# Kernel optimization log

Hardware: AMD Instinct MI355X
Metric: run time of the kernel (lower is better)

## Reference

```python
import jax, jax.numpy as jnp
import numpy as np

N, E, H, NH = 10000, 160000, 128, 8
HD = H // NH
LDIM = 8  # (lmax+1)**2 - 1 with lmax=2
CUTOFF = 5.0


def setup_inputs() -> dict:
    key = jax.random.key(0)
    ks = jax.random.split(key, 20)
    w = lambda k, shape: jax.random.normal(k, shape, jnp.float32) * 0.05
    return dict(
        node_feats=jax.random.normal(ks[0], (N, H), jnp.float32),
        edge_feats=jax.random.normal(ks[1], (E, H), jnp.float32),
        vector_feats=jax.random.normal(ks[2], (N, LDIM, H), jnp.float32),
        distances=jax.random.uniform(ks[3], (E,), jnp.float32) * CUTOFF,
        d_ij=jax.random.normal(ks[4], (E, LDIM), jnp.float32),
        senders=jax.random.randint(ks[5], (E,), 0, N),
        receivers=jax.random.randint(ks[6], (E,), 0, N),
        ln_scale=jnp.ones((H,), jnp.float32),
        ln_bias=jnp.zeros((H,), jnp.float32),
        vln_w=jnp.ones((H,), jnp.float32),
        W_vec=w(ks[7], (H, 3 * H)),
        Wq=w(ks[8], (H, H)), bq=jnp.zeros((H,), jnp.float32),
        Wk=w(ks[9], (H, H)), bk=jnp.zeros((H,), jnp.float32),
        Wv=w(ks[10], (H, H)), bv=jnp.zeros((H,), jnp.float32),
        Wdk=w(ks[11], (H, H)), bdk=jnp.zeros((H,), jnp.float32),
        Wdv=w(ks[12], (H, H)), bdv=jnp.zeros((H,), jnp.float32),
        Ws=w(ks[13], (H, 2 * H)), bs=jnp.zeros((2 * H,), jnp.float32),
        Wo=w(ks[14], (H, 3 * H)), bo=jnp.zeros((3 * H,), jnp.float32),
        Wf=w(ks[15], (H, H)), bf=jnp.zeros((H,), jnp.float32),
        Wsrc=w(ks[16], (H, H)),
        Wtrg=w(ks[17], (H, H)),
    )


def _reject(vec, d):
    # vector rejection of vec [E, L, H] against direction d [E, L]
    proj = (vec * d[:, :, None]).sum(axis=1, keepdims=True)
    return vec - proj * d[:, :, None]


def _forward(node_feats, edge_feats, vector_feats, distances, d_ij, senders, receivers,
             ln_scale, ln_bias, vln_w, W_vec, Wq, bq, Wk, bk, Wv, bv, Wdk, bdk, Wdv, bdv,
             Ws, bs, Wo, bo, Wf, bf, Wsrc, Wtrg):
    silu = jax.nn.silu
    n = node_feats.shape[0]
    # LayerNorm (eps=1e-5) on node feats
    mu = node_feats.mean(-1, keepdims=True)
    xc = node_feats - mu
    var = (xc * xc).mean(-1, keepdims=True)
    x = xc * jax.lax.rsqrt(var + 1e-5) * ln_scale + ln_bias
    # VecLayerNorm with norm_type='none' -> identity norm + learned per-channel scale
    vec = vector_feats * vln_w
    q = (x @ Wq + bq).reshape(-1, NH, HD)
    k = (x @ Wk + bk).reshape(-1, NH, HD)
    v = (x @ Wv + bv).reshape(-1, NH, HD)
    dk = silu(edge_feats @ Wdk + bdk).reshape(-1, NH, HD)
    dv = silu(edge_feats @ Wdv + bdv).reshape(-1, NH, HD)
    vec1, vec2, vec3 = jnp.split(vec @ W_vec, [H, 2 * H], axis=-1)
    vec_dot = (vec1 * vec2).sum(axis=1)  # [N, H]
    # per-edge gathers
    q_i = q[receivers]
    k_j = k[senders]
    v_j = v[senders]
    vec_j = vec[senders]  # [E, LDIM, H]
    # attention-style message with cosine cutoff
    cut = 0.5 * (jnp.cos(distances * (jnp.pi / CUTOFF)) + 1.0) * (distances < CUTOFF)
    attn = silu((q_i * k_j * dk).sum(-1)) * cut[:, None]  # [E, NH]
    vj = ((v_j * dv) * attn[:, :, None]).reshape(-1, H)   # [E, H]
    s1, s2 = jnp.split(silu(vj @ Ws + bs), [H], axis=1)
    vec_msg = vec_j * s1[:, None, :] + s2[:, None, :] * d_ij[:, :, None]
    # scatter reduce to nodes
    node_agg = jax.ops.segment_sum(vj, receivers, num_segments=n)
    vec_agg = jax.ops.segment_sum(vec_msg, receivers, num_segments=n)
    o1, o2, o3 = jnp.split(node_agg @ Wo + bo, [H, 2 * H], axis=1)
    dx = vec_dot * o2 + o3
    dvec = vec3 * o1[:, None, :] + vec_agg
    # edge update (last_layer=False)
    w1 = _reject(vec[receivers] @ Wtrg, d_ij)
    w2 = _reject(vec_j @ Wsrc, -d_ij)
    w_dot = (w1 * w2).sum(axis=1)  # [E, H]
    df_ij = silu(edge_feats @ Wf + bf) * w_dot
    return dx, df_ij, dvec


def reference(node_feats, edge_feats, vector_feats, distances, d_ij, senders, receivers,
              ln_scale, ln_bias, vln_w, W_vec, Wq, bq, Wk, bk, Wv, bv, Wdk, bdk, Wdv, bdv,
              Ws, bs, Wo, bo, Wf, bf, Wsrc, Wtrg):
    return _forward(node_feats, edge_feats, vector_feats, distances, d_ij, senders, receivers,
                    ln_scale, ln_bias, vln_w, W_vec, Wq, bq, Wk, bk, Wv, bv, Wdk, bdk, Wdv, bdv,
                    Ws, bs, Wo, bo, Wf, bf, Wsrc, Wtrg)
```

## Files before the change

### kernel.cpp

```cpp
#include <hip/hip_runtime.h>
#include <math.h>

#define NN 10000
#define NE 160000
#define H  128
#define LD 8

typedef unsigned short ushort_t;
typedef short bf16x8 __attribute__((ext_vector_type(8)));
typedef float f32x4 __attribute__((ext_vector_type(4)));

__device__ __forceinline__ float silu_f(float x){ return x / (1.0f + expf(-x)); }
__device__ __forceinline__ float4 f4z(){ return make_float4(0.f,0.f,0.f,0.f); }

__device__ __forceinline__ ushort_t f2bf(float f){
    union { float f; unsigned int u; } x; x.f = f;
    unsigned int r = x.u + 0x7FFFu + ((x.u >> 16) & 1u);
    return (ushort_t)(r >> 16);
}
__device__ __forceinline__ unsigned int pack2bf(float a, float b){
    return (unsigned int)f2bf(a) | ((unsigned int)f2bf(b) << 16);
}
__device__ __forceinline__ float bf2f_hi(unsigned int u){
    union { unsigned int u; float f; } x; x.u = u & 0xffff0000u; return x.f;
}
__device__ __forceinline__ float bf2f_lo(unsigned int u){
    union { unsigned int u; float f; } x; x.u = u << 16; return x.f;
}
__device__ __forceinline__ float bfu2f(ushort_t u){
    union { unsigned int u; float f; } x; x.u = ((unsigned int)u) << 16; return x.f;
}

__global__ void k_prepw(const float* __restrict__ Wq, const float* __restrict__ Wk,
                        const float* __restrict__ Wv, const float* __restrict__ W_vec,
                        const float* __restrict__ Wtrg, const float* __restrict__ Wsrc,
                        const float* __restrict__ Wdk, const float* __restrict__ Wdv,
                        const float* __restrict__ Ws,  const float* __restrict__ Wf,
                        ushort_t* __restrict__ wqkvT, ushort_t* __restrict__ wvecT,
                        ushort_t* __restrict__ wdkT, ushort_t* __restrict__ wdvT,
                        ushort_t* __restrict__ wsT,
                        ushort_t* __restrict__ wfT_hi, ushort_t* __restrict__ wfT_lo){
    int i = blockIdx.x * 256 + threadIdx.x;
    int n = i >> 7, kk = i & 127;
    if (n < 384){
        float v;
        if (n < 128)      v = Wq[kk*128 + n];
        else if (n < 256) v = Wk[kk*128 + (n-128)];
        else              v = Wv[kk*128 + (n-256)];
        wqkvT[n*128 + kk] = f2bf(v);
    } else if (n < 1024){
        int m = n - 384;
        float v;
        if (m < 384)      v = W_vec[kk*384 + m];
        else if (m < 512) v = Wtrg[kk*128 + (m-384)];
        else              v = Wsrc[kk*128 + (m-512)];
        wvecT[m*128 + kk] = f2bf(v);
    } else if (n < 1152){
        int m = n - 1024;
        wdkT[m*128 + kk] = f2bf(Wdk[kk*128 + m]);
    } else if (n < 1280){
        int m = n - 1152;
        wdvT[m*128 + kk] = f2bf(Wdv[kk*128 + m]);
    } else if (n < 1536){
        int m = n - 1280;
        wsT[m*128 + kk] = f2bf(Ws[kk*256 + m]);
    } else if (n < 1664){
        int m = n - 1536;
        float v = Wf[kk*128 + m];
        ushort_t hi = f2bf(v);
        wfT_hi[m*128 + kk] = hi;
        wfT_lo[m*128 + kk] = f2bf(v - bfu2f(hi));
    }
}

__global__ void k_hist(const int* __restrict__ rcv, int* __restrict__ cnt){
    int e = blockIdx.x * 256 + threadIdx.x;
    if (e < NE) atomicAdd(&cnt[rcv[e]], 1);
}

__global__ __launch_bounds__(256) void k_scan(const int* __restrict__ cnt, int* __restrict__ offs){
    __shared__ int part[256];
    const int t = threadIdx.x;
    const int CH = 40;
    int loc[CH];
    int base = t * CH;
    int lsum = 0;
    if (base < NN){
        #pragma unroll
        for (int i = 0; i < CH; i++){ loc[i] = cnt[base + i]; lsum += loc[i]; }
    }
    part[t] = lsum;
    __syncthreads();
    for (int off = 1; off < 256; off <<= 1){
        int v = (t >= off) ? part[t - off] : 0;
        __syncthreads();
        part[t] += v;
        __syncthreads();
    }
    int ex = part[t] - lsum;
    if (base < NN){
        int run = ex;
        #pragma unroll
        for (int i = 0; i < CH; i++){ offs[base + i] = run; run += loc[i]; }
    }
    if (t == 255) offs[NN] = part[255];
}

__global__ void k_scatter(const int* __restrict__ rcv, const int* __restrict__ offs,
                          int* __restrict__ cnt2, int* __restrict__ eidx){
    int e = blockIdx.x * 256 + threadIdx.x;
    if (e < NE){
        int r = rcv[e];
        int p = atomicAdd(&cnt2[r], 1);
        eidx[offs[r] + p] = e;
    }
}

__global__ __launch_bounds__(256) void k_perm(
    const float* __restrict__ ef, const int* __restrict__ eidx,
    const int* __restrict__ snd, const int* __restrict__ rcv,
    const float* __restrict__ dist, const float* __restrict__ dij,
    float* __restrict__ ef_srt, ushort_t* __restrict__ ef_bf_srt,
    int* __restrict__ snd_srt, int* __restrict__ rcv_srt,
    float* __restrict__ dist_srt, float* __restrict__ dij_srt)
{
    __shared__ int eidx_s[64];
    const int tid = threadIdx.x;
    const int p0  = blockIdx.x * 64;
    if (tid < 64){
        int p = p0 + tid;
        int e = eidx[p];
        eidx_s[tid] = e;
        snd_srt[p]  = snd[e];
        rcv_srt[p]  = rcv[e];
        dist_srt[p] = dist[e];
    }
    __syncthreads();
    const int r = tid >> 2, cq = tid & 3;
    const int e = eidx_s[r];
    const int p = p0 + r;
    const float4* src = (const float4*)(ef + (size_t)e*H + cq*32);
    float4* dst  = (float4*)(ef_srt + (size_t)p*H + cq*32);
    ushort_t* db = ef_bf_srt + (size_t)p*H + cq*32;
    #pragma unroll
    for (int j = 0; j < 8; j++){
        float4 v = src[j];
        dst[j] = v;
        uint2 u; u.x = pack2bf(v.x, v.y); u.y = pack2bf(v.z, v.w);
        *(uint2*)(db + j*4) = u;
    }
    if (cq == 0){
        *(float4*)(dij_srt + (size_t)p*LD)     = *(const float4*)(dij + (size_t)e*LD);
        *(float4*)(dij_srt + (size_t)p*LD + 4) = *(const float4*)(dij + (size_t)e*LD + 4);
    }
}

__global__ __launch_bounds__(128) void node_ln(
    const float* __restrict__ nf, const float* __restrict__ vf,
    const float* __restrict__ ln_s, const float* __restrict__ ln_b,
    const float* __restrict__ vlnw,
    ushort_t* __restrict__ x_bf, ushort_t* __restrict__ vec_bf)
{
    const int n = blockIdx.x, h = threadIdx.x;
    __shared__ float red[4];
    float xv = nf[(size_t)n*H + h];
    float s1 = xv, s2 = xv*xv;
    #pragma unroll
    for (int o = 32; o >= 1; o >>= 1){
        s1 += __shfl_xor(s1, o, 64);
        s2 += __shfl_xor(s2, o, 64);
    }
    const int wid = h >> 6;
    if ((h & 63) == 0){ red[wid] = s1; red[2+wid] = s2; }
    __syncthreads();
    float mean = (red[0] + red[1]) * (1.0f/H);
    float var  = (red[2] + red[3]) * (1.0f/H) - mean*mean;
    float x = (xv - mean) * rsqrtf(var + 1e-5f) * ln_s[h] + ln_b[h];
    x_bf[(size_t)n*H + h] = f2bf(x);
    float w = vlnw[h];
    #pragma unroll
    for (int l = 0; l < LD; l++){
        size_t i = ((size_t)n*LD + l)*H + h;
        vec_bf[i] = f2bf(vf[i] * w);
    }
}

__global__ __launch_bounds__(256) void node_qkv(
    const ushort_t* __restrict__ x_bf, const ushort_t* __restrict__ wqkvT,
    const float* __restrict__ bq, const float* __restrict__ bk, const float* __restrict__ bv,
    float* __restrict__ q, float* __restrict__ k, float* __restrict__ v)
{
    const int tid  = threadIdx.x;
    const int lane = tid & 63;
    const int m0   = (tid >> 6) * 16;
    const int e0   = blockIdx.x * 64;

    const int mrow = lane & 15;
    const int kblk = lane >> 4;

    f32x4 acc[24];
    #pragma unroll
    for (int nt = 0; nt < 24; nt++) acc[nt] = (f32x4)(0.f);

    int arow = e0 + m0 + mrow; if (arow >= NN) arow = NN-1;
    const ushort_t* Arow = x_bf + (size_t)arow*H + kblk*8;
    const ushort_t* wb   = wqkvT + (size_t)mrow*H + kblk*8;

    #pragma unroll
    for (int ks = 0; ks < 4; ks++){
        bf16x8 a = *(const bf16x8*)(Arow + ks*32);
        #pragma unroll
        for (int nt = 0; nt < 24; nt++){
            bf16x8 b8 = *(const bf16x8*)(wb + (size_t)nt*16*H + ks*32);
            acc[nt] = __builtin_amdgcn_mfma_f32_16x16x32_bf16(a, b8, acc[nt], 0, 0, 0);
        }
    }
    float* outs[3] = {q, k, v};
    const float* bias[3] = {bq, bk, bv};
    #pragma unroll
    for (int g = 0; g < 3; g++){
        #pragma unroll
        for (int t = 0; t < 8; t++){
            int col = t*16 + mrow;
            float bb = bias[g][col];
            #pragma unroll
            for (int r = 0; r < 4; r++){
                int row = e0 + m0 + kblk*4 + r;
                if (row < NN) outs[g][(size_t)row*H + col] = acc[g*8+t][r] + bb;
            }
        }
    }
}

__global__ __launch_bounds__(256) void node_vec(
    const ushort_t* __restrict__ vec_bf, const ushort_t* __restrict__ wvecT,
    float* __restrict__ vdot, ushort_t* __restrict__ vec3,
    ushort_t* __restrict__ Vt, ushort_t* __restrict__ Vs)
{
    __shared__ ushort_t st_s[64][136];

    const int tid  = threadIdx.x;
    const int lane = tid & 63;
    const int wv   = tid >> 6;
    const int m0   = wv * 16;
    const size_t r0 = (size_t)blockIdx.x * 64;

    const int mrow = lane & 15;
    const int kblk = lane >> 4;

    f32x4 acc[40];
    #pragma unroll
    for (int nt = 0; nt < 40; nt++) acc[nt] = (f32x4)(0.f);

    const ushort_t* Arow = vec_bf + (r0 + m0 + mrow)*H + kblk*8;
    const ushort_t* wb   = wvecT + (size_t)mrow*H + kblk*8;

    #pragma unroll
    for (int ks = 0; ks < 4; ks++){
        bf16x8 a = *(const bf16x8*)(Arow + ks*32);
        #pragma unroll
        for (int nt = 0; nt < 40; nt++){
            bf16x8 b8 = *(const bf16x8*)(wb + (size_t)nt*16*H + ks*32);
            acc[nt] = __builtin_amdgcn_mfma_f32_16x16x32_bf16(a, b8, acc[nt], 0, 0, 0);
        }
    }

    #pragma unroll
    for (int t = 0; t < 8; t++){
        float p = acc[t][0]*acc[t+8][0] + acc[t][1]*acc[t+8][1]
                + acc[t][2]*acc[t+8][2] + acc[t][3]*acc[t+8][3];
        p += __shfl_xor(p, 16, 64);
        if ((kblk & 1) == 0){
            int node = (int)(r0 >> 3) + wv*2 + (kblk >> 1);
            vdot[(size_t)node*H + t*16 + mrow] = p;
        }
    }

    ushort_t* outs[3] = {vec3, Vt, Vs};
    #pragma unroll
    for (int g = 0; g < 3; g++){
        __syncthreads();
        #pragma unroll
        for (int t = 0; t < 8; t++){
            int coln = t*16 + mrow;
            int lr = m0 + kblk*4;
            st_s[lr+0][coln] = f2bf(acc[16+g*8+t][0]);
            st_s[lr+1][coln] = f2bf(acc[16+g*8+t][1]);
            st_s[lr+2][coln] = f2bf(acc[16+g*8+t][2]);
            st_s[lr+3][coln] = f2bf(acc[16+g*8+t][3]);
        }
        __syncthreads();
        const int rr = tid >> 2, qq = tid & 3;
        uint4* dst = (uint4*)&outs[g][(r0 + rr)*H + qq*32];
        const uint4* src = (const uint4*)&st_s[rr][qq*32];
        dst[0] = src[0]; dst[1] = src[1]; dst[2] = src[2]; dst[3] = src[3];
    }
}

__global__ __launch_bounds__(256) void edge_attn(
    const ushort_t* __restrict__ ef_bf,
    const ushort_t* __restrict__ wdkT, const float* __restrict__ bdk,
    const ushort_t* __restrict__ wdvT, const float* __restrict__ bdv,
    const int* __restrict__ snd_srt, const int* __restrict__ rcv_srt,
    const float* __restrict__ dist_srt,
    const float* __restrict__ q, const float* __restrict__ k, const float* __restrict__ v,
    ushort_t* __restrict__ vj)
{
    __shared__ ushort_t dk_s[64][136];
    __shared__ ushort_t dv_s[64][136];

    const int tid  = threadIdx.x;
    const int lane = tid & 63;
    const int m0   = (tid >> 6) * 16;
    const size_t e0 = (size_t)blockIdx.x * 64;

    const int mrow = lane & 15;
    const int kblk = lane >> 4;

    f32x4 accK[8], accV[8];
    #pragma unroll
    for (int nt = 0; nt < 8; nt++){ accK[nt] = (f32x4)(0.f); accV[nt] = (f32x4)(0.f); }

    const ushort_t* Arow = ef_bf + (e0 + m0 + mrow)*H + kblk*8;
    const ushort_t* wkb  = wdkT + (size_t)mrow*H + kblk*8;
    const ushort_t* wvb  = wdvT + (size_t)mrow*H + kblk*8;

    #pragma unroll
    for (int ks = 0; ks < 4; ks++){
        bf16x8 a = *(const bf16x8*)(Arow + ks*32);
        #pragma unroll
        for (int nt = 0; nt < 8; nt++){
            bf16x8 bk8 = *(const bf16x8*)(wkb + (size_t)nt*16*H + ks*32);
            accK[nt] = __builtin_amdgcn_mfma_f32_16x16x32_bf16(a, bk8, accK[nt], 0, 0, 0);
            bf16x8 bv8 = *(const bf16x8*)(wvb + (size_t)nt*16*H + ks*32);
            accV[nt] = __builtin_amdgcn_mfma_f32_16x16x32_bf16(a, bv8, accV[nt], 0, 0, 0);
        }
    }

    const int lrow = m0 + 4*kblk;
    #pragma unroll
    for (int nt = 0; nt < 8; nt++){
        int coln = nt*16 + mrow;
        float bkn = bdk[coln], bvn = bdv[coln];
        #pragma unroll
        for (int r = 0; r < 4; r++){
            dk_s[lrow + r][coln] = f2bf(silu_f(accK[nt][r] + bkn));
            dv_s[lrow + r][coln] = f2bf(silu_f(accV[nt][r] + bvn));
        }
    }
    __syncthreads();

    const int r  = tid >> 2, cq = tid & 3;
    const size_t e = e0 + r;
    const int s  = snd_srt[e], rr = rcv_srt[e];
    const float d = dist_srt[e];
    const float cut = (d < 5.0f) ? 0.5f*(cosf(d*0.6283185307179586f) + 1.0f) : 0.0f;
    const float* qrow = q + (size_t)rr*H + cq*32;
    const float* krow = k + (size_t)s*H + cq*32;
    const float* vrow = v + (size_t)s*H + cq*32;
    ushort_t* vjrow = vj + e*H + cq*32;

    #pragma unroll
    for (int hh = 0; hh < 2; hh++){
        const int c0 = hh*16;
        float p = 0.f;
        #pragma unroll
        for (int j = 0; j < 4; j++){
            float4 q4 = *(const float4*)(qrow + c0 + 4*j);
            float4 k4 = *(const float4*)(krow + c0 + 4*j);
            uint2 du = *(const uint2*)&dk_s[r][cq*32 + c0 + 4*j];
            p += q4.x*k4.x*bf2f_lo(du.x) + q4.y*k4.y*bf2f_hi(du.x)
               + q4.z*k4.z*bf2f_lo(du.y) + q4.w*k4.w*bf2f_hi(du.y);
        }
        float attn = silu_f(p) * cut;
        #pragma unroll
        for (int j = 0; j < 4; j++){
            float4 v4 = *(const float4*)(vrow + c0 + 4*j);
            uint2 du = *(const uint2*)&dv_s[r][cq*32 + c0 + 4*j];
            uint2 u;
            u.x = pack2bf(v4.x*bf2f_lo(du.x)*attn, v4.y*bf2f_hi(du.x)*attn);
            u.y = pack2bf(v4.z*bf2f_lo(du.y)*attn, v4.w*bf2f_hi(du.y)*attn);
            *(uint2*)(vjrow + c0 + 4*j) = u;
        }
    }
}

__global__ __launch_bounds__(256) void edge_s(
    const ushort_t* __restrict__ vj, const ushort_t* __restrict__ wsT,
    const float* __restrict__ bs, ushort_t* __restrict__ s12)
{
    __shared__ ushort_t s_s[64][264];

    const int tid  = threadIdx.x;
    const int lane = tid & 63;
    const int m0   = (tid >> 6) * 16;
    const size_t e0 = (size_t)blockIdx.x * 64;

    const int mrow = lane & 15;
    const int kblk = lane >> 4;

    f32x4 acc[16];
    #pragma unroll
    for (int nt = 0; nt < 16; nt++) acc[nt] = (f32x4)(0.f);

    const ushort_t* Arow = vj + (e0 + m0 + mrow)*H + kblk*8;
    const ushort_t* wb   = wsT + (size_t)mrow*H + kblk*8;

    #pragma unroll
    for (int ks = 0; ks < 4; ks++){
        bf16x8 a = *(const bf16x8*)(Arow + ks*32);
        #pragma unroll
        for (int nt = 0; nt < 16; nt++){
            bf16x8 b8 = *(const bf16x8*)(wb + (size_t)nt*16*H + ks*32);
            acc[nt] = __builtin_amdgcn_mfma_f32_16x16x32_bf16(a, b8, acc[nt], 0, 0, 0);
        }
    }

    const int lrow = m0 + 4*kblk;
    #pragma unroll
    for (int nt = 0; nt < 16; nt++){
        int coln = nt*16 + mrow;
        float bb = bs[coln];
        #pragma unroll
        for (int r = 0; r < 4; r++)
            s_s[lrow + r][coln] = f2bf(silu_f(acc[nt][r] + bb));
    }
    __syncthreads();

    const int r = tid >> 2, cq = tid & 3;
    const uint4* srcp = (const uint4*)&s_s[r][cq*64];
    uint4* dstp = (uint4*)&s12[(e0 + r)*256 + cq*64];
    #pragma unroll
    for (int j = 0; j < 8; j++) dstp[j] = srcp[j];
}

__global__ __launch_bounds__(256) void edge_f(
    const float* __restrict__ ef,
    const ushort_t* __restrict__ wfT_hi, const ushort_t* __restrict__ wfT_lo,
    const float* __restrict__ bf_, float* __restrict__ f)
{
    const int tid  = threadIdx.x;
    const int lane = tid & 63;
    const int m0   = (tid >> 6) * 16;
    const size_t e0 = (size_t)blockIdx.x * 64;

    const int mrow = lane & 15;
    const int kblk = lane >> 4;

    f32x4 acc[8];
    #pragma unroll
    for (int nt = 0; nt < 8; nt++) acc[nt] = (f32x4)(0.f);

    const float* Arow = ef + (e0 + m0 + mrow)*H + kblk*8;
    const ushort_t* wh = wfT_hi + (size_t)mrow*H + kblk*8;
    const ushort_t* wl = wfT_lo + (size_t)mrow*H + kblk*8;

    #pragma unroll
    for (int ks = 0; ks < 4; ks++){
        float4 v0 = *(const float4*)(Arow + ks*32);
        float4 v1 = *(const float4*)(Arow + ks*32 + 4);
        float vv[8] = {v0.x, v0.y, v0.z, v0.w, v1.x, v1.y, v1.z, v1.w};
        union { short s[8]; bf16x8 v; } ah, al;
        #pragma unroll
        for (int j = 0; j < 8; j++){
            ushort_t hi = f2bf(vv[j]);
            ah.s[j] = (short)hi;
            al.s[j] = (short)f2bf(vv[j] - bfu2f(hi));
        }
        #pragma unroll
        for (int nt = 0; nt < 8; nt++){
            bf16x8 bh = *(const bf16x8*)(wh + (size_t)nt*16*H + ks*32);
            bf16x8 bl = *(const bf16x8*)(wl + (size_t)nt*16*H + ks*32);
            acc[nt] = __builtin_amdgcn_mfma_f32_16x16x32_bf16(ah.v, bh, acc[nt], 0, 0, 0);
            acc[nt] = __builtin_amdgcn_mfma_f32_16x16x32_bf16(al.v, bh, acc[nt], 0, 0, 0);
            acc[nt] = __builtin_amdgcn_mfma_f32_16x16x32_bf16(ah.v, bl, acc[nt], 0, 0, 0);
            acc[nt] = __builtin_amdgcn_mfma_f32_16x16x32_bf16(al.v, bl, acc[nt], 0, 0, 0);
        }
    }

    #pragma unroll
    for (int nt = 0; nt < 8; nt++){
        int col = nt*16 + mrow;
        float bb = bf_[col];
        #pragma unroll
        for (int r = 0; r < 4; r++)
            f[(e0 + m0 + 4*kblk + r)*H + col] = silu_f(acc[nt][r] + bb);
    }
}

__global__ __launch_bounds__(512) void node_fuse(
    const int* __restrict__ offs, const int* __restrict__ eidx,
    const int* __restrict__ snd_srt,
    const ushort_t* __restrict__ vj, const ushort_t* __restrict__ s12,
    const float* __restrict__ dij_srt, const ushort_t* __restrict__ vec,
    const float* __restrict__ f,
    const ushort_t* __restrict__ Vt, const ushort_t* __restrict__ Vs,
    const float* __restrict__ Wo, const float* __restrict__ bo,
    const float* __restrict__ vdot, const ushort_t* __restrict__ vec3,
    float* __restrict__ dx, float* __restrict__ df, float* __restrict__ dvec)
{
    const int n = blockIdx.x;
    const int tid = threadIdx.x;
    const int h = tid & 127;
    const int par = tid >> 7;
    const int beg = offs[n], end = offs[n+1];

    float AT[LD];
    {
        const ushort_t* At = Vt + (size_t)n*LD*H + h;
        #pragma unroll
        for (int l = 0; l < LD; l++) AT[l] = bfu2f(At[l*H]);
    }

    float na = 0.f;
    float av[LD];
    #pragma unroll
    for (int l = 0; l < LD; l++) av[l] = 0.f;

    for (int i = beg + par; i < end; i += 4){
        int s = snd_srt[i];
        float vjv = bf2f_lo((unsigned int)vj[(size_t)i*H + h]);
        float s1 = bf2f_lo((unsigned int)s12[(size_t)i*256 + h]);
        float s2 = bf2f_lo((unsigned int)s12[(size_t)i*256 + 128 + h]);
        na += vjv;
        float4 d0 = *(const float4*)&dij_srt[(size_t)i*LD];
        float4 d1 = *(const float4*)&dij_srt[(size_t)i*LD + 4];
        float dl[LD];
        dl[0]=d0.x; dl[1]=d0.y; dl[2]=d0.z; dl[3]=d0.w;
        dl[4]=d1.x; dl[5]=d1.y; dl[6]=d1.z; dl[7]=d1.w;
        float dd = 0.f;
        #pragma unroll
        for (int l = 0; l < LD; l++) dd = fmaf(dl[l], dl[l], dd);
        const float c2 = 2.0f - dd;

        const ushort_t* vr = &vec[(size_t)s*LD*H + h];
        const ushort_t* Bs = &Vs[(size_t)s*LD*H + h];
        float AB = 0.f, aa_ = 0.f, bb_ = 0.f;
        #pragma unroll
        for (int l = 0; l < LD; l++){
            float vv = bfu2f(vr[l*H]);
            float Bl = bfu2f(Bs[l*H]);
            av[l] = fmaf(vv, s1, fmaf(dl[l], s2, av[l]));
            AB  = fmaf(AT[l], Bl, AB);
            aa_ = fmaf(AT[l], dl[l], aa_);
            bb_ = fmaf(Bl, dl[l], bb_);
        }
        float fv = f[(size_t)i*H + h];
        df[(size_t)eidx[i]*H + h] = fv * (AB - aa_*bb_*c2);
    }

    __shared__ float pl[4][LD+1][128];
    __shared__ float o_s[3][128];
    #pragma unroll
    for (int l = 0; l < LD; l++) pl[par][l][h] = av[l];
    pl[par][LD][h] = na;
    __syncthreads();

    if (par == 0){
        #pragma unroll
        for (int l = 0; l <= LD; l++)
            pl[0][l][h] = (pl[0][l][h] + pl[1][l][h]) + (pl[2][l][h] + pl[3][l][h]);
    }
    __syncthreads();

    if (par > 0){
        const int g = par - 1;
        float o = bo[g*H + h];
        for (int kk = 0; kk < H; kk++)
            o = fmaf(pl[0][LD][kk], Wo[kk*(3*H) + g*H + h], o);
        o_s[g][h] = o;
    }
    __syncthreads();

    if (par == 0){
        dx[(size_t)n*H + h] = fmaf(vdot[(size_t)n*H + h], o_s[1][h], o_s[2][h]);
        #pragma unroll
        for (int l = 0; l < LD; l++){
            size_t i2 = ((size_t)n*LD + l)*H + h;
            dvec[i2] = fmaf(bf2f_lo((unsigned int)vec3[i2]), o_s[0][h], pl[0][l][h]);
        }
    }
}

extern "C" void kernel_launch(void* const* d_in, const int* in_sizes, int n_in,
                              void* d_out, int out_size, void* d_ws, size_t ws_size,
                              hipStream_t stream) {
    const float* nf    = (const float*)d_in[0];
    const float* ef    = (const float*)d_in[1];
    const float* vf    = (const float*)d_in[2];
    const float* dist  = (const float*)d_in[3];
    const float* dij   = (const float*)d_in[4];
    const int*   snd   = (const int*)d_in[5];
    const int*   rcv   = (const int*)d_in[6];
    const float* ln_s  = (const float*)d_in[7];
    const float* ln_b  = (const float*)d_in[8];
    const float* vlnw  = (const float*)d_in[9];
    const float* W_vec = (const float*)d_in[10];
    const float* Wq    = (const float*)d_in[11];
    const float* bq    = (const float*)d_in[12];
    const float* Wk    = (const float*)d_in[13];
    const float* bk    = (const float*)d_in[14];
    const float* Wv    = (const float*)d_in[15];
    const float* bv    = (const float*)d_in[16];
    const float* Wdk   = (const float*)d_in[17];
    const float* bdk   = (const float*)d_in[18];
    const float* Wdv   = (const float*)d_in[19];
    const float* bdv   = (const float*)d_in[20];
    const float* Ws    = (const float*)d_in[21];
    const float* bs    = (const float*)d_in[22];
    const float* Wo    = (const float*)d_in[23];
    const float* bo    = (const float*)d_in[24];
    const float* Wf    = (const float*)d_in[25];
    const float* bf_   = (const float*)d_in[26];
    const float* Wsrc  = (const float*)d_in[27];
    const float* Wtrg  = (const float*)d_in[28];

    float* out  = (float*)d_out;
    float* dx   = out;
    float* df   = out + (size_t)NN*H;
    float* dvec = df + (size_t)NE*H;

    float* w = (float*)d_ws;
    size_t off = 0;
    float* q    = w + off; off += (size_t)NN*H;
    float* k    = w + off; off += (size_t)NN*H;
    float* v    = w + off; off += (size_t)NN*H;
    float* vdot = w + off; off += (size_t)NN*H;
    ushort_t* x_bf   = (ushort_t*)(w + off); off += (size_t)NN*H/2;
    ushort_t* vec_bf = (ushort_t*)(w + off); off += (size_t)NN*LD*H/2;
    ushort_t* vec3   = (ushort_t*)(w + off); off += (size_t)NN*LD*H/2;
    ushort_t* Vt     = (ushort_t*)(w + off); off += (size_t)NN*LD*H/2;
    ushort_t* Vs     = (ushort_t*)(w + off); off += (size_t)NN*LD*H/2;
    ushort_t* vj     = (ushort_t*)(w + off); off += (size_t)NE*H/2;
    float*    ef_srt = (float*)(w + off);
    ushort_t* s12    = (ushort_t*)(w + off); off += (size_t)NE*H;
    ushort_t* ef_bf_srt = (ushort_t*)(w + off);
    float*    f         = (float*)(w + off); off += (size_t)NE*H;
    ushort_t* wqkvT  = (ushort_t*)(w + off); off += 384*128/2;
    ushort_t* wvecT  = (ushort_t*)(w + off); off += 640*128/2;
    ushort_t* wdkT   = (ushort_t*)(w + off); off += 128*128/2;
    ushort_t* wdvT   = (ushort_t*)(w + off); off += 128*128/2;
    ushort_t* wsT    = (ushort_t*)(w + off); off += 256*128/2;
    ushort_t* wfT_hi = (ushort_t*)(w + off); off += 128*128/2;
    ushort_t* wfT_lo = (ushort_t*)(w + off); off += 128*128/2;
    int* cnt  = (int*)(w + off); off += NN;
    int* cnt2 = (int*)(w + off); off += NN;
    int* offs = (int*)(w + off); off += NN + 1;
    int* eidx = (int*)(w + off); off += NE;
    int* snd_srt = (int*)(w + off); off += NE;
    int* rcv_srt = (int*)(w + off); off += NE;
    float* dist_srt = (float*)(w + off); off += NE;
    float* dij_srt  = (float*)(w + off); off += (size_t)NE*LD;

    hipMemsetAsync(cnt,  0, NN*sizeof(int), stream);
    hipMemsetAsync(cnt2, 0, NN*sizeof(int), stream);

    k_prepw<<<832, 256, 0, stream>>>(Wq, Wk, Wv, W_vec, Wtrg, Wsrc, Wdk, Wdv, Ws, Wf,
                                     wqkvT, wvecT, wdkT, wdvT, wsT, wfT_hi, wfT_lo);

    k_hist<<<(NE+255)/256, 256, 0, stream>>>(rcv, cnt);
    k_scan<<<1, 256, 0, stream>>>(cnt, offs);
    k_scatter<<<(NE+255)/256, 256, 0, stream>>>(rcv, offs, cnt2, eidx);

    k_perm<<<NE/64, 256, 0, stream>>>(ef, eidx, snd, rcv, dist, dij,
                                      ef_srt, ef_bf_srt, snd_srt, rcv_srt,
                                      dist_srt, dij_srt);

    node_ln<<<NN, 128, 0, stream>>>(nf, vf, ln_s, ln_b, vlnw, x_bf, vec_bf);

    node_qkv<<<(NN+63)/64, 256, 0, stream>>>(x_bf, wqkvT, bq, bk, bv, q, k, v);

    node_vec<<<NN*LD/64, 256, 0, stream>>>(vec_bf, wvecT, vdot, vec3, Vt, Vs);

    edge_attn<<<NE/64, 256, 0, stream>>>(ef_bf_srt, wdkT, bdk, wdvT, bdv,
                                         snd_srt, rcv_srt, dist_srt, q, k, v, vj);

    edge_f<<<NE/64, 256, 0, stream>>>(ef_srt, wfT_hi, wfT_lo, bf_, f);

    edge_s<<<NE/64, 256, 0, stream>>>(vj, wsT, bs, s12);

    node_fuse<<<NN, 512, 0, stream>>>(offs, eidx, snd_srt, vj, s12, dij_srt, vec_bf,
                                      f, Vt, Vs, Wo, bo, vdot, vec3, dx, df, dvec);
}
```

Before: 905.8 us.

## Transpose per-node vector tensors to h-major and store gathered K/V in bf16

Vector features and the Vt/Vs projections are now also written in a [node][h][l] layout, so node_fuse fetches all 8 l-components of a gathered sender row with one 16-byte load instead of 8 strided 2-byte loads. The s1/s2 gates are interleaved into one 32-bit word per channel. K and V are stored as bf16 to halve the bytes gathered per edge in edge_attn. The costs are an extra vec_t write, less coalesced transposed stores in node_vec, and reduced precision for K and V.

```diff
diff --git a/kernel.cpp b/kernel.cpp
--- a/kernel.cpp
+++ b/kernel.cpp
@@ -159,7 +159,8 @@
     const float* __restrict__ nf, const float* __restrict__ vf,
     const float* __restrict__ ln_s, const float* __restrict__ ln_b,
     const float* __restrict__ vlnw,
-    ushort_t* __restrict__ x_bf, ushort_t* __restrict__ vec_bf)
+    ushort_t* __restrict__ x_bf, ushort_t* __restrict__ vec_bf,
+    ushort_t* __restrict__ vec_t)
 {
     const int n = blockIdx.x, h = threadIdx.x;
     __shared__ float red[4];
@@ -178,17 +179,21 @@
     float x = (xv - mean) * rsqrtf(var + 1e-5f) * ln_s[h] + ln_b[h];
     x_bf[(size_t)n*H + h] = f2bf(x);
     float w = vlnw[h];
+    union { ushort_t s[8]; uint4 u; } pk;
     #pragma unroll
     for (int l = 0; l < LD; l++){
         size_t i = ((size_t)n*LD + l)*H + h;
-        vec_bf[i] = f2bf(vf[i] * w);
-    }
+        ushort_t b = f2bf(vf[i] * w);
+        vec_bf[i] = b;
+        pk.s[l] = b;
+    }
+    *(uint4*)&vec_t[((size_t)n*H + h)*8] = pk.u;
 }
 
 __global__ __launch_bounds__(256) void node_qkv(
     const ushort_t* __restrict__ x_bf, const ushort_t* __restrict__ wqkvT,
     const float* __restrict__ bq, const float* __restrict__ bk, const float* __restrict__ bv,
-    float* __restrict__ q, float* __restrict__ k, float* __restrict__ v)
+    float* __restrict__ q, ushort_t* __restrict__ k_bf, ushort_t* __restrict__ v_bf)
 {
     const int tid  = threadIdx.x;
     const int lane = tid & 63;
@@ -215,19 +220,34 @@
             acc[nt] = __builtin_amdgcn_mfma_f32_16x16x32_bf16(a, b8, acc[nt], 0, 0, 0);
         }
     }
-    float* outs[3] = {q, k, v};
-    const float* bias[3] = {bq, bk, bv};
-    #pragma unroll
-    for (int g = 0; g < 3; g++){
-        #pragma unroll
-        for (int t = 0; t < 8; t++){
-            int col = t*16 + mrow;
-            float bb = bias[g][col];
-            #pragma unroll
-            for (int r = 0; r < 4; r++){
-                int row = e0 + m0 + kblk*4 + r;
-                if (row < NN) outs[g][(size_t)row*H + col] = acc[g*8+t][r] + bb;
-            }
+    #pragma unroll
+    for (int t = 0; t < 8; t++){
+        int col = t*16 + mrow;
+        float bb = bq[col];
+        #pragma unroll
+        for (int r = 0; r < 4; r++){
+            int row = e0 + m0 + kblk*4 + r;
+            if (row < NN) q[(size_t)row*H + col] = acc[t][r] + bb;
+        }
+    }
+    #pragma unroll
+    for (int t = 0; t < 8; t++){
+        int col = t*16 + mrow;
+        float bb = bk[col];
+        #pragma unroll
+        for (int r = 0; r < 4; r++){
+            int row = e0 + m0 + kblk*4 + r;
+            if (row < NN) k_bf[(size_t)row*H + col] = f2bf(acc[8+t][r] + bb);
+        }
+    }
+    #pragma unroll
+    for (int t = 0; t < 8; t++){
+        int col = t*16 + mrow;
+        float bb = bv[col];
+        #pragma unroll
+        for (int r = 0; r < 4; r++){
+            int row = e0 + m0 + kblk*4 + r;
+            if (row < NN) v_bf[(size_t)row*H + col] = f2bf(acc[16+t][r] + bb);
         }
     }
 }
@@ -235,7 +255,7 @@
 __global__ __launch_bounds__(256) void node_vec(
     const ushort_t* __restrict__ vec_bf, const ushort_t* __restrict__ wvecT,
     float* __restrict__ vdot, ushort_t* __restrict__ vec3,
-    ushort_t* __restrict__ Vt, ushort_t* __restrict__ Vs)
+    ushort_t* __restrict__ Vt_t, ushort_t* __restrict__ Vs_t)
 {
     __shared__ ushort_t st_s[64][136];
 
@@ -276,24 +296,48 @@
         }
     }
 
-    ushort_t* outs[3] = {vec3, Vt, Vs};
-    #pragma unroll
-    for (int g = 0; g < 3; g++){
+    __syncthreads();
+    #pragma unroll
+    for (int t = 0; t < 8; t++){
+        int coln = t*16 + mrow;
+        int lr = m0 + kblk*4;
+        st_s[lr+0][coln] = f2bf(acc[16+t][0]);
+        st_s[lr+1][coln] = f2bf(acc[16+t][1]);
+        st_s[lr+2][coln] = f2bf(acc[16+t][2]);
+        st_s[lr+3][coln] = f2bf(acc[16+t][3]);
+    }
+    __syncthreads();
+    {
+        const int rr = tid >> 2, qq = tid & 3;
+        uint4* dst = (uint4*)&vec3[(r0 + rr)*H + qq*32];
+        const uint4* src = (const uint4*)&st_s[rr][qq*32];
+        dst[0] = src[0]; dst[1] = src[1]; dst[2] = src[2]; dst[3] = src[3];
+    }
+
+    #pragma unroll
+    for (int g = 0; g < 2; g++){
         __syncthreads();
+        const int base = 24 + g*8;
         #pragma unroll
         for (int t = 0; t < 8; t++){
             int coln = t*16 + mrow;
             int lr = m0 + kblk*4;
-            st_s[lr+0][coln] = f2bf(acc[16+g*8+t][0]);
-            st_s[lr+1][coln] = f2bf(acc[16+g*8+t][1]);
-            st_s[lr+2][coln] = f2bf(acc[16+g*8+t][2]);
-            st_s[lr+3][coln] = f2bf(acc[16+g*8+t][3]);
+            st_s[lr+0][coln] = f2bf(acc[base+t][0]);
+            st_s[lr+1][coln] = f2bf(acc[base+t][1]);
+            st_s[lr+2][coln] = f2bf(acc[base+t][2]);
+            st_s[lr+3][coln] = f2bf(acc[base+t][3]);
         }
         __syncthreads();
-        const int rr = tid >> 2, qq = tid & 3;
-        uint4* dst = (uint4*)&outs[g][(r0 + rr)*H + qq*32];
-        const uint4* src = (const uint4*)&st_s[rr][qq*32];
-        dst[0] = src[0]; dst[1] = src[1]; dst[2] = src[2]; dst[3] = src[3];
+        ushort_t* dstb = (g == 0) ? Vt_t : Vs_t;
+        #pragma unroll
+        for (int j = 0; j < 4; j++){
+            int p = tid + 256*j;
+            int nl = p >> 7, hh = p & 127;
+            union { ushort_t s[8]; uint4 u; } pk;
+            #pragma unroll
+            for (int l = 0; l < 8; l++) pk.s[l] = st_s[nl*8 + l][hh];
+            *(uint4*)&dstb[(((r0 >> 3) + nl)*(size_t)H + hh)*8] = pk.u;
+        }
     }
 }
 
@@ -303,7 +347,8 @@
     const ushort_t* __restrict__ wdvT, const float* __restrict__ bdv,
     const int* __restrict__ snd_srt, const int* __restrict__ rcv_srt,
     const float* __restrict__ dist_srt,
-    const float* __restrict__ q, const float* __restrict__ k, const float* __restrict__ v,
+    const float* __restrict__ q, const ushort_t* __restrict__ k_bf,
+    const ushort_t* __restrict__ v_bf,
     ushort_t* __restrict__ vj)
 {
     __shared__ ushort_t dk_s[64][136];
@@ -355,9 +400,9 @@
     const int s  = snd_srt[e], rr = rcv_srt[e];
     const float d = dist_srt[e];
     const float cut = (d < 5.0f) ? 0.5f*(cosf(d*0.6283185307179586f) + 1.0f) : 0.0f;
-    const float* qrow = q + (size_t)rr*H + cq*32;
-    const float* krow = k + (size_t)s*H + cq*32;
-    const float* vrow = v + (size_t)s*H + cq*32;
+    const float*    qrow = q    + (size_t)rr*H + cq*32;
+    const ushort_t* krow = k_bf + (size_t)s*H + cq*32;
+    const ushort_t* vrow = v_bf + (size_t)s*H + cq*32;
     ushort_t* vjrow = vj + e*H + cq*32;
 
     #pragma unroll
@@ -367,19 +412,21 @@
         #pragma unroll
         for (int j = 0; j < 4; j++){
             float4 q4 = *(const float4*)(qrow + c0 + 4*j);
-            float4 k4 = *(const float4*)(krow + c0 + 4*j);
+            uint2 ku = *(const uint2*)(krow + c0 + 4*j);
             uint2 du = *(const uint2*)&dk_s[r][cq*32 + c0 + 4*j];
-            p += q4.x*k4.x*bf2f_lo(du.x) + q4.y*k4.y*bf2f_hi(du.x)
-               + q4.z*k4.z*bf2f_lo(du.y) + q4.w*k4.w*bf2f_hi(du.y);
+            p += q4.x*bf2f_lo(ku.x)*bf2f_lo(du.x) + q4.y*bf2f_hi(ku.x)*bf2f_hi(du.x)
+               + q4.z*bf2f_lo(ku.y)*bf2f_lo(du.y) + q4.w*bf2f_hi(ku.y)*bf2f_hi(du.y);
         }
         float attn = silu_f(p) * cut;
         #pragma unroll
         for (int j = 0; j < 4; j++){
-            float4 v4 = *(const float4*)(vrow + c0 + 4*j);
+            uint2 vu = *(const uint2*)(vrow + c0 + 4*j);
             uint2 du = *(const uint2*)&dv_s[r][cq*32 + c0 + 4*j];
             uint2 u;
-            u.x = pack2bf(v4.x*bf2f_lo(du.x)*attn, v4.y*bf2f_hi(du.x)*attn);
-            u.y = pack2bf(v4.z*bf2f_lo(du.y)*attn, v4.w*bf2f_hi(du.y)*attn);
+            u.x = pack2bf(bf2f_lo(vu.x)*bf2f_lo(du.x)*attn,
+                          bf2f_hi(vu.x)*bf2f_hi(du.x)*attn);
+            u.y = pack2bf(bf2f_lo(vu.y)*bf2f_lo(du.y)*attn,
+                          bf2f_hi(vu.y)*bf2f_hi(du.y)*attn);
             *(uint2*)(vjrow + c0 + 4*j) = u;
         }
     }
@@ -387,7 +434,7 @@
 
 __global__ __launch_bounds__(256) void edge_s(
     const ushort_t* __restrict__ vj, const ushort_t* __restrict__ wsT,
-    const float* __restrict__ bs, ushort_t* __restrict__ s12)
+    const float* __restrict__ bs, unsigned int* __restrict__ s12p)
 {
     __shared__ ushort_t s_s[64][264];
 
@@ -428,10 +475,16 @@
     __syncthreads();
 
     const int r = tid >> 2, cq = tid & 3;
-    const uint4* srcp = (const uint4*)&s_s[r][cq*64];
-    uint4* dstp = (uint4*)&s12[(e0 + r)*256 + cq*64];
-    #pragma unroll
-    for (int j = 0; j < 8; j++) dstp[j] = srcp[j];
+    #pragma unroll
+    for (int j = 0; j < 8; j++){
+        int hh = cq*32 + j*4;
+        uint4 o;
+        o.x = (unsigned)s_s[r][hh+0] | ((unsigned)s_s[r][128+hh+0] << 16);
+        o.y = (unsigned)s_s[r][hh+1] | ((unsigned)s_s[r][128+hh+1] << 16);
+        o.z = (unsigned)s_s[r][hh+2] | ((unsigned)s_s[r][128+hh+2] << 16);
+        o.w = (unsigned)s_s[r][hh+3] | ((unsigned)s_s[r][128+hh+3] << 16);
+        *(uint4*)&s12p[(e0 + r)*H + hh] = o;
+    }
 }
 
 __global__ __launch_bounds__(256) void edge_f(
@@ -491,10 +544,10 @@
 __global__ __launch_bounds__(512) void node_fuse(
     const int* __restrict__ offs, const int* __restrict__ eidx,
     const int* __restrict__ snd_srt,
-    const ushort_t* __restrict__ vj, const ushort_t* __restrict__ s12,
-    const float* __restrict__ dij_srt, const ushort_t* __restrict__ vec,
+    const ushort_t* __restrict__ vj, const unsigned int* __restrict__ s12p,
+    const float* __restrict__ dij_srt, const ushort_t* __restrict__ vec_t,
     const float* __restrict__ f,
-    const ushort_t* __restrict__ Vt, const ushort_t* __restrict__ Vs,
+    const ushort_t* __restrict__ Vt_t, const ushort_t* __restrict__ Vs_t,
     const float* __restrict__ Wo, const float* __restrict__ bo,
     const float* __restrict__ vdot, const ushort_t* __restrict__ vec3,
     float* __restrict__ dx, float* __restrict__ df, float* __restrict__ dvec)
@@ -507,9 +560,11 @@
 
     float AT[LD];
     {
-        const ushort_t* At = Vt + (size_t)n*LD*H + h;
-        #pragma unroll
-        for (int l = 0; l < LD; l++) AT[l] = bfu2f(At[l*H]);
+        uint4 ut = *(const uint4*)&Vt_t[((size_t)n*H + h)*8];
+        AT[0]=bf2f_lo(ut.x); AT[1]=bf2f_hi(ut.x);
+        AT[2]=bf2f_lo(ut.y); AT[3]=bf2f_hi(ut.y);
+        AT[4]=bf2f_lo(ut.z); AT[5]=bf2f_hi(ut.z);
+        AT[6]=bf2f_lo(ut.w); AT[7]=bf2f_hi(ut.w);
     }
 
     float na = 0.f;
@@ -519,9 +574,9 @@
 
     for (int i = beg + par; i < end; i += 4){
         int s = snd_srt[i];
-        float vjv = bf2f_lo((unsigned int)vj[(size_t)i*H + h]);
-        float s1 = bf2f_lo((unsigned int)s12[(size_t)i*256 + h]);
-        float s2 = bf2f_lo((unsigned int)s12[(size_t)i*256 + 128 + h]);
+        float vjv = bfu2f(vj[(size_t)i*H + h]);
+        unsigned p12 = s12p[(size_t)i*H + h];
+        float s1 = bf2f_lo(p12), s2 = bf2f_hi(p12);
         na += vjv;
         float4 d0 = *(const float4*)&dij_srt[(size_t)i*LD];
         float4 d1 = *(const float4*)&dij_srt[(size_t)i*LD + 4];
@@ -533,17 +588,21 @@
         for (int l = 0; l < LD; l++) dd = fmaf(dl[l], dl[l], dd);
         const float c2 = 2.0f - dd;
 
-        const ushort_t* vr = &vec[(size_t)s*LD*H + h];
-        const ushort_t* Bs = &Vs[(size_t)s*LD*H + h];
+        uint4 uv = *(const uint4*)&vec_t[((size_t)s*H + h)*8];
+        uint4 ub = *(const uint4*)&Vs_t[((size_t)s*H + h)*8];
+        float vvx[LD], Blx[LD];
+        vvx[0]=bf2f_lo(uv.x); vvx[1]=bf2f_hi(uv.x); vvx[2]=bf2f_lo(uv.y); vvx[3]=bf2f_hi(uv.y);
+        vvx[4]=bf2f_lo(uv.z); vvx[5]=bf2f_hi(uv.z); vvx[6]=bf2f_lo(uv.w); vvx[7]=bf2f_hi(uv.w);
+        Blx[0]=bf2f_lo(ub.x); Blx[1]=bf2f_hi(ub.x); Blx[2]=bf2f_lo(ub.y); Blx[3]=bf2f_hi(ub.y);
+        Blx[4]=bf2f_lo(ub.z); Blx[5]=bf2f_hi(ub.z); Blx[6]=bf2f_lo(ub.w); Blx[7]=bf2f_hi(ub.w);
+
         float AB = 0.f, aa_ = 0.f, bb_ = 0.f;
         #pragma unroll
         for (int l = 0; l < LD; l++){
-            float vv = bfu2f(vr[l*H]);
-            float Bl = bfu2f(Bs[l*H]);
-            av[l] = fmaf(vv, s1, fmaf(dl[l], s2, av[l]));
-            AB  = fmaf(AT[l], Bl, AB);
+            av[l] = fmaf(vvx[l], s1, fmaf(dl[l], s2, av[l]));
+            AB  = fmaf(AT[l], Blx[l], AB);
             aa_ = fmaf(AT[l], dl[l], aa_);
-            bb_ = fmaf(Bl, dl[l], bb_);
+            bb_ = fmaf(Blx[l], dl[l], bb_);
         }
         float fv = f[(size_t)i*H + h];
         df[(size_t)eidx[i]*H + h] = fv * (AB - aa_*bb_*c2);
@@ -577,7 +636,7 @@
         #pragma unroll
         for (int l = 0; l < LD; l++){
             size_t i2 = ((size_t)n*LD + l)*H + h;
-            dvec[i2] = fmaf(bf2f_lo((unsigned int)vec3[i2]), o_s[0][h], pl[0][l][h]);
+            dvec[i2] = fmaf(bfu2f(vec3[i2]), o_s[0][h], pl[0][l][h]);
         }
     }
 }
@@ -623,17 +682,18 @@
     float* w = (float*)d_ws;
     size_t off = 0;
     float* q    = w + off; off += (size_t)NN*H;
-    float* k    = w + off; off += (size_t)NN*H;
-    float* v    = w + off; off += (size_t)NN*H;
     float* vdot = w + off; off += (size_t)NN*H;
+    ushort_t* k_bf   = (ushort_t*)(w + off); off += (size_t)NN*H/2;
+    ushort_t* v_bf   = (ushort_t*)(w + off); off += (size_t)NN*H/2;
     ushort_t* x_bf   = (ushort_t*)(w + off); off += (size_t)NN*H/2;
     ushort_t* vec_bf = (ushort_t*)(w + off); off += (size_t)NN*LD*H/2;
+    ushort_t* vec_t  = (ushort_t*)(w + off); off += (size_t)NN*LD*H/2;
     ushort_t* vec3   = (ushort_t*)(w + off); off += (size_t)NN*LD*H/2;
-    ushort_t* Vt     = (ushort_t*)(w + off); off += (size_t)NN*LD*H/2;
-    ushort_t* Vs     = (ushort_t*)(w + off); off += (size_t)NN*LD*H/2;
+    ushort_t* Vt_t   = (ushort_t*)(w + off); off += (size_t)NN*LD*H/2;
+    ushort_t* Vs_t   = (ushort_t*)(w + off); off += (size_t)NN*LD*H/2;
     ushort_t* vj     = (ushort_t*)(w + off); off += (size_t)NE*H/2;
-    float*    ef_srt = (float*)(w + off);
-    ushort_t* s12    = (ushort_t*)(w + off); off += (size_t)NE*H;
+    float*        ef_srt = (float*)(w + off);
+    unsigned int* s12p   = (unsigned int*)(w + off); off += (size_t)NE*H;
     ushort_t* ef_bf_srt = (ushort_t*)(w + off);
     float*    f         = (float*)(w + off); off += (size_t)NE*H;
     ushort_t* wqkvT  = (ushort_t*)(w + off); off += 384*128/2;
@@ -666,19 +726,19 @@
                                       ef_srt, ef_bf_srt, snd_srt, rcv_srt,
                                       dist_srt, dij_srt);
 
-    node_ln<<<NN, 128, 0, stream>>>(nf, vf, ln_s, ln_b, vlnw, x_bf, vec_bf);
-
-    node_qkv<<<(NN+63)/64, 256, 0, stream>>>(x_bf, wqkvT, bq, bk, bv, q, k, v);
-
-    node_vec<<<NN*LD/64, 256, 0, stream>>>(vec_bf, wvecT, vdot, vec3, Vt, Vs);
+    node_ln<<<NN, 128, 0, stream>>>(nf, vf, ln_s, ln_b, vlnw, x_bf, vec_bf, vec_t);
+
+    node_qkv<<<(NN+63)/64, 256, 0, stream>>>(x_bf, wqkvT, bq, bk, bv, q, k_bf, v_bf);
+
+    node_vec<<<NN*LD/64, 256, 0, stream>>>(vec_bf, wvecT, vdot, vec3, Vt_t, Vs_t);
 
     edge_attn<<<NE/64, 256, 0, stream>>>(ef_bf_srt, wdkT, bdk, wdvT, bdv,
-                                         snd_srt, rcv_srt, dist_srt, q, k, v, vj);
+                                         snd_srt, rcv_srt, dist_srt, q, k_bf, v_bf, vj);
 
     edge_f<<<NE/64, 256, 0, stream>>>(ef_srt, wfT_hi, wfT_lo, bf_, f);
 
-    edge_s<<<NE/64, 256, 0, stream>>>(vj, wsT, bs, s12);
-
-    node_fuse<<<NN, 512, 0, stream>>>(offs, eidx, snd_srt, vj, s12, dij_srt, vec_bf,
-                                      f, Vt, Vs, Wo, bo, vdot, vec3, dx, df, dvec);
-}
+    edge_s<<<NE/64, 256, 0, stream>>>(vj, wsT, bs, s12p);
+
+    node_fuse<<<NN, 512, 0, stream>>>(offs, eidx, snd_srt, vj, s12p, dij_srt, vec_t,
+                                      f, Vt_t, Vs_t, Wo, bo, vdot, vec3, dx, df, dvec);
+}
```

Measured after the change: 883.8 us. 1.02x faster.
